# Performance work log

Measured on AMD Instinct MI355X. Metric: run time of the kernel, lower is better.

The kernel has to match this reference:

```python
import jax, jax.numpy as jnp
import numpy as np

B, Q, LE, D, P, A = 8, 32, 128, 512, 32, 128


def setup_inputs() -> dict:
    key = jax.random.key(0)
    ks = jax.random.split(key, 8)
    exp_tokens = jax.random.normal(ks[0], (B, Q, LE, D), dtype=jnp.float32)
    exp_mask = jax.random.randint(ks[1], (B, Q, LE), 0, 2, dtype=jnp.int32)
    s_j = jax.random.normal(ks[2], (B, P, D), dtype=jnp.float32)
    req_mask = jax.random.randint(ks[3], (B, P), 0, 2, dtype=jnp.int32)
    sc = 1.0 / np.sqrt(D)
    Ws_w = jax.random.normal(ks[4], (A, D), dtype=jnp.float32) * sc
    Ws_b = jax.random.normal(ks[5], (A,), dtype=jnp.float32) * 0.01
    U_w = jax.random.normal(ks[6], (A, D), dtype=jnp.float32) * sc
    v_w = jax.random.normal(ks[7], (1, A), dtype=jnp.float32) * (1.0 / np.sqrt(A))
    return {"exp_tokens": exp_tokens, "exp_mask": exp_mask, "s_j": s_j,
            "req_mask": req_mask, "Ws_w": Ws_w, "Ws_b": Ws_b, "U_w": U_w, "v_w": v_w}


def reference(exp_tokens, exp_mask, s_j, req_mask, Ws_w, Ws_b, U_w, v_w):
    # ws: (B,P,A); uh: (B,Q,Le,A)
    ws = jnp.einsum('bpd,ad->bpa', s_j, Ws_w) + Ws_b
    uh = jnp.einsum('bqtd,ad->bqta', exp_tokens, U_w)
    # broadcast add -> (B,Q,P,Le,A), tanh, project with v -> (B,Q,P,Le)
    scored = jnp.tanh(uh[:, :, None, :, :] + ws[:, None, :, None, :])
    e = jnp.einsum('bqpta,a->bqpt', scored, v_w[0])
    tok_mask = exp_mask[:, :, None, :]  # (B,Q,1,Le) broadcast over P
    e = jnp.where(tok_mask == 0, jnp.float32(-1e9), e)
    # joint softmax over Q*Le per (b,p)
    e_t = jnp.transpose(e, (0, 2, 1, 3)).reshape(e.shape[0], e.shape[2], -1)
    a = jax.nn.softmax(e_t, axis=-1).reshape(e.shape[0], e.shape[2], e.shape[1], e.shape[3])
    a = jnp.transpose(a, (0, 2, 1, 3))  # (B,Q,P,Le)
    s_rlk = jnp.einsum('bqpt,bqtd->bqpd', a, exp_tokens)
    rmask = req_mask[:, None, :, None].astype(s_rlk.dtype)
    return s_rlk * rmask
```

## Files before the change

### kernel.cpp

```cpp
#include <hip/hip_runtime.h>
#include <hip/hip_bf16.h>

#define B_  8
#define Q_  32
#define LE_ 128
#define D_  512
#define P_  32
#define A_  128

typedef __attribute__((ext_vector_type(8))) short short8_t;
typedef __attribute__((ext_vector_type(4))) float floatx4_t;

typedef const __attribute__((address_space(1))) unsigned int glb_uint;
typedef __attribute__((address_space(3))) unsigned int lds_uint;
#define GLD16(g, s) __builtin_amdgcn_global_load_lds((glb_uint*)(g), (lds_uint*)(s), 16, 0, 0)

__device__ __forceinline__ short f2bf(float x) {
    unsigned u = __float_as_uint(x);
    unsigned r = (u + 0x7fffu + ((u >> 16) & 1u)) >> 16;
    return (short)r;
}
__device__ __forceinline__ float bf2f(short s) {
    return __uint_as_float(((unsigned)(unsigned short)s) << 16);
}

__global__ __launch_bounds__(256) void convert_kernel(
    const float* __restrict__ X, const float* __restrict__ W,
    short* __restrict__ Xb, short* __restrict__ Wb) {
    int b = blockIdx.x;
    const float* src;
    short* dst;
    size_t base;
    if (b < 8192) {
        base = ((size_t)b * 256 + threadIdx.x) * 8;
        src = X + base; dst = Xb + base;
    } else {
        base = ((size_t)(b - 8192) * 256 + threadIdx.x) * 8;
        src = W + base; dst = Wb + base;
    }
    float4 v0 = ((const float4*)src)[0];
    float4 v1 = ((const float4*)src)[1];
    short8_t s;
    s[0] = f2bf(v0.x); s[1] = f2bf(v0.y); s[2] = f2bf(v0.z); s[3] = f2bf(v0.w);
    s[4] = f2bf(v1.x); s[5] = f2bf(v1.y); s[6] = f2bf(v1.z); s[7] = f2bf(v1.w);
    *(short8_t*)dst = s;
}

__global__ __launch_bounds__(128) void ws_kernel(
    const float* __restrict__ s_j, const float* __restrict__ Ws_w,
    const float* __restrict__ Ws_b, float* __restrict__ ws) {
    __shared__ float s_row[D_];
    int bp = blockIdx.x;
    const float* src = s_j + (size_t)bp * D_;
    for (int i = threadIdx.x; i < D_; i += 128) s_row[i] = src[i];
    __syncthreads();
    int a = threadIdx.x;
    const float4* w4 = (const float4*)(Ws_w + (size_t)a * D_);
    const float4* s4 = (const float4*)s_row;
    float acc = 0.0f;
#pragma unroll 8
    for (int i = 0; i < D_ / 4; ++i) {
        float4 w = w4[i];
        float4 s = s4[i];
        acc += w.x * s.x + w.y * s.y + w.z * s.z + w.w * s.w;
    }
    ws[bp * A_ + a] = __expf(2.0f * (acc + Ws_b[a]));
}

#define EUP_ 136
#define EWP_ 132
#define WPP_ 136

__global__ __launch_bounds__(512, 1) void fused_kernel(
    const short* __restrict__ Xb, const short* __restrict__ Wb,
    const float* __restrict__ EW, const float* __restrict__ v_w,
    const int* __restrict__ exp_mask, float* __restrict__ gsums,
    float* __restrict__ out) {
    __shared__ short uA[128 * EUP_];
    __shared__ float ew_s[32 * EWP_];
    __shared__ short w_s[32 * WPP_];
    __shared__ float n2v[128];
    __shared__ int   mask_s[128];

    int bq = blockIdx.x;
    int b  = bq >> 5;
    int tid = threadIdx.x;
    int wave = tid >> 6, lane = tid & 63;
    int qd = lane >> 4, lr = lane & 15;

    short* As = uA;
    short* Bs = uA + 8192;

    int m0 = (wave >> 1) * 32, n0 = (wave & 1) * 64;
    int cA = lane & 7;
    int row0 = wave * 16 + (lane >> 3);

    floatx4_t acc[2][4];
#pragma unroll
    for (int i = 0; i < 2; ++i)
#pragma unroll
        for (int j = 0; j < 4; ++j) acc[i][j] = (floatx4_t){0.f, 0.f, 0.f, 0.f};

    for (int kt = 0; kt < 8; ++kt) {
        int k0 = kt * 64;
        __syncthreads();
#pragma unroll
        for (int u = 0; u < 2; ++u) {
            int m = row0 + u * 8;
            GLD16(Xb + (size_t)(bq * 128 + m) * D_ + k0 + ((cA ^ (m & 7)) * 8),
                  As + (wave * 2 + u) * 512);
        }
#pragma unroll
        for (int u = 0; u < 2; ++u) {
            int n = row0 + u * 8;
            GLD16(Wb + (size_t)n * D_ + k0 + ((cA ^ (n & 7)) * 8),
                  Bs + (wave * 2 + u) * 512);
        }
        __syncthreads();
#pragma unroll
        for (int ks = 0; ks < 2; ++ks) {
            int cr = (ks * 4 + qd) ^ (lr & 7);
            short8_t af[2], bfr[4];
#pragma unroll
            for (int i = 0; i < 2; ++i)
                af[i] = *(const short8_t*)(As + (m0 + i * 16 + lr) * 64 + cr * 8);
#pragma unroll
            for (int j = 0; j < 4; ++j)
                bfr[j] = *(const short8_t*)(Bs + (n0 + j * 16 + lr) * 64 + cr * 8);
#pragma unroll
            for (int i = 0; i < 2; ++i)
#pragma unroll
                for (int j = 0; j < 4; ++j)
                    acc[i][j] = __builtin_amdgcn_mfma_f32_16x16x32_bf16(af[i], bfr[j], acc[i][j], 0, 0, 0);
        }
    }
    __syncthreads();

#pragma unroll
    for (int i = 0; i < 2; ++i)
#pragma unroll
        for (int j = 0; j < 4; ++j)
#pragma unroll
            for (int r = 0; r < 4; ++r) {
                int t = m0 + i * 16 + qd * 4 + r;
                int a = n0 + j * 16 + lr;
                uA[t * EUP_ + a] = f2bf(__expf(2.0f * acc[i][j][r]));
            }
#pragma unroll
    for (int u = 0; u < 2; ++u) {
        int c = tid * 2 + u;
        int p = c >> 5, seg = c & 31;
        *(float4*)&ew_s[p * EWP_ + seg * 4] =
            *(const float4*)&EW[(size_t)(b * P_ + p) * A_ + seg * 4];
    }
    if (tid < 32) {
        float4 v = *(const float4*)(v_w + tid * 4);
        v.x *= -2.0f; v.y *= -2.0f; v.z *= -2.0f; v.w *= -2.0f;
        *(float4*)&n2v[tid * 4] = v;
    }
    if (tid < 128) mask_s[tid] = exp_mask[bq * LE_ + tid];
    __syncthreads();

    {
        int t = tid & 127, pg = tid >> 7;
        float acc8[8];
#pragma unroll
        for (int j = 0; j < 8; ++j) acc8[j] = 0.0f;
        for (int a8 = 0; a8 < 16; ++a8) {
            short8_t e8 = *(const short8_t*)&uA[t * EUP_ + a8 * 8];
            float eu[8];
#pragma unroll
            for (int k = 0; k < 8; ++k) eu[k] = bf2f(e8[k]);
            float4 nv0 = *(const float4*)&n2v[a8 * 8];
            float4 nv1 = *(const float4*)&n2v[a8 * 8 + 4];
            float nv[8] = {nv0.x, nv0.y, nv0.z, nv0.w, nv1.x, nv1.y, nv1.z, nv1.w};
#pragma unroll
            for (int j = 0; j < 8; ++j) {
                int p = pg * 8 + j;
                float4 w0 = *(const float4*)&ew_s[p * EWP_ + a8 * 8];
                float4 w1 = *(const float4*)&ew_s[p * EWP_ + a8 * 8 + 4];
                float ww[8] = {w0.x, w0.y, w0.z, w0.w, w1.x, w1.y, w1.z, w1.w};
#pragma unroll
                for (int k = 0; k < 8; ++k)
                    acc8[j] = fmaf(nv[k], __builtin_amdgcn_rcpf(fmaf(eu[k], ww[k], 1.0f)), acc8[j]);
            }
        }
        int mk = mask_s[t];
#pragma unroll
        for (int j = 0; j < 8; ++j) {
            float ee = mk ? __expf(acc8[j]) : 0.0f;
            w_s[(pg * 8 + j) * WPP_ + t] = f2bf(ee);
        }
    }
    __syncthreads();

    if (tid < 256) {
        int p = tid >> 3, seg = tid & 7;
        const short* src = w_s + p * WPP_ + seg * 16;
        float s = 0.0f;
#pragma unroll
        for (int k = 0; k < 16; ++k) s += bf2f(src[k]);
        s += __shfl_xor(s, 1);
        s += __shfl_xor(s, 2);
        s += __shfl_xor(s, 4);
        if (seg == 0) atomicAdd(&gsums[b * P_ + p], s);
    }

    short8_t afv[2][4];
#pragma unroll
    for (int i = 0; i < 2; ++i)
#pragma unroll
        for (int ks = 0; ks < 4; ++ks)
            afv[i][ks] = *(const short8_t*)&w_s[(i * 16 + lr) * WPP_ + ks * 32 + qd * 8];

    int tt = tid >> 2, dseg = (tid & 3) * 32;
    for (int chunk = 0; chunk < 4; ++chunk) {
        int d0 = chunk * 128;
        __syncthreads();
        const short8_t* g = (const short8_t*)(Xb + (size_t)(bq * 128 + tt) * D_ + d0 + dseg);
        short8_t xs0 = g[0], xs1 = g[1], xs2 = g[2], xs3 = g[3];
#pragma unroll
        for (int e = 0; e < 8; ++e) {
            uA[(dseg + 0 + e) * EUP_ + tt]  = xs0[e];
            uA[(dseg + 8 + e) * EUP_ + tt]  = xs1[e];
            uA[(dseg + 16 + e) * EUP_ + tt] = xs2[e];
            uA[(dseg + 24 + e) * EUP_ + tt] = xs3[e];
        }
        __syncthreads();
        floatx4_t accp[2];
        accp[0] = (floatx4_t){0.f, 0.f, 0.f, 0.f};
        accp[1] = (floatx4_t){0.f, 0.f, 0.f, 0.f};
#pragma unroll
        for (int ks = 0; ks < 4; ++ks) {
            short8_t bfr = *(const short8_t*)&uA[(wave * 16 + lr) * EUP_ + ks * 32 + qd * 8];
            accp[0] = __builtin_amdgcn_mfma_f32_16x16x32_bf16(afv[0][ks], bfr, accp[0], 0, 0, 0);
            accp[1] = __builtin_amdgcn_mfma_f32_16x16x32_bf16(afv[1][ks], bfr, accp[1], 0, 0, 0);
        }
#pragma unroll
        for (int i = 0; i < 2; ++i)
#pragma unroll
            for (int r = 0; r < 4; ++r) {
                int p = i * 16 + qd * 4 + r;
                out[((size_t)bq * P_ + p) * D_ + d0 + wave * 16 + lr] = accp[i][r];
            }
    }
}

__global__ __launch_bounds__(256) void norm_kernel(
    float* __restrict__ out, const float* __restrict__ gsums,
    const int* __restrict__ req_mask) {
    int bqp = blockIdx.x;
    int p = bqp & 31;
    int b = bqp >> 10;
    int bp = b * P_ + p;
    float s = gsums[bp];
    float rm = req_mask[bp] ? __fdividef(1.0f, s) : 0.0f;
    float2* o = (float2*)(out + (size_t)bqp * D_);
    float2 v = o[threadIdx.x];
    v.x *= rm; v.y *= rm;
    o[threadIdx.x] = v;
}

extern "C" void kernel_launch(void* const* d_in, const int* in_sizes, int n_in,
                              void* d_out, int out_size, void* d_ws, size_t ws_size,
                              hipStream_t stream) {
    const float* exp_tokens = (const float*)d_in[0];
    const int*   exp_mask   = (const int*)d_in[1];
    const float* s_j        = (const float*)d_in[2];
    const int*   req_mask   = (const int*)d_in[3];
    const float* Ws_w       = (const float*)d_in[4];
    const float* Ws_b       = (const float*)d_in[5];
    const float* U_w        = (const float*)d_in[6];
    const float* v_w        = (const float*)d_in[7];
    float* out = (float*)d_out;

    float* EW    = (float*)d_ws;
    float* gsums = EW + B_ * P_ * A_;
    short* Xb    = (short*)(gsums + 256);
    short* Wb    = Xb + (size_t)B_ * Q_ * LE_ * D_;

    hipMemsetAsync(gsums, 0, B_ * P_ * sizeof(float), stream);
    convert_kernel<<<dim3(8192 + 32), dim3(256), 0, stream>>>(exp_tokens, U_w, Xb, Wb);
    ws_kernel<<<dim3(B_ * P_), dim3(128), 0, stream>>>(s_j, Ws_w, Ws_b, EW);
    fused_kernel<<<dim3(B_ * Q_), dim3(512), 0, stream>>>(Xb, Wb, EW, v_w, exp_mask, gsums, out);
    norm_kernel<<<dim3(B_ * Q_ * P_), dim3(256), 0, stream>>>(out, gsums, req_mask);
}
```

Before: 169.6 us.

## Fuse normalization into main kernel via cooperative grid sync

Removes the separate norm kernel: the fused kernel now performs a grid-wide cooperative sync after all blocks accumulate softmax denominators, reads the per-(b,p) sums, and scales the output by the reciprocal times the request mask before writing. Output stores become nontemporal. This saves a kernel launch and a full read-modify-write pass over the output, at the cost of a grid barrier that requires all 256 blocks to be co-resident.

```diff
diff --git a/kernel.cpp b/kernel.cpp
--- a/kernel.cpp
+++ b/kernel.cpp
@@ -1,5 +1,6 @@
 #include <hip/hip_runtime.h>
 #include <hip/hip_bf16.h>
+#include <hip/hip_cooperative_groups.h>
 
 #define B_  8
 #define Q_  32
@@ -75,7 +76,7 @@
     const short* __restrict__ Xb, const short* __restrict__ Wb,
     const float* __restrict__ EW, const float* __restrict__ v_w,
     const int* __restrict__ exp_mask, float* __restrict__ gsums,
-    float* __restrict__ out) {
+    const int* __restrict__ req_mask, float* __restrict__ out) {
     __shared__ short uA[128 * EUP_];
     __shared__ float ew_s[32 * EWP_];
     __shared__ short w_s[32 * WPP_];
@@ -213,6 +214,14 @@
         for (int ks = 0; ks < 4; ++ks)
             afv[i][ks] = *(const short8_t*)&w_s[(i * 16 + lr) * WPP_ + ks * 32 + qd * 8];
 
+    cooperative_groups::this_grid().sync();
+
+    if (tid < 32) {
+        int bp = b * P_ + tid;
+        float g = atomicAdd(&gsums[bp], 0.0f);
+        n2v[tid] = req_mask[bp] ? __builtin_amdgcn_rcpf(g) : 0.0f;
+    }
+
     int tt = tid >> 2, dseg = (tid & 3) * 32;
     for (int chunk = 0; chunk < 4; ++chunk) {
         int d0 = chunk * 128;
@@ -241,24 +250,12 @@
 #pragma unroll
             for (int r = 0; r < 4; ++r) {
                 int p = i * 16 + qd * 4 + r;
-                out[((size_t)bq * P_ + p) * D_ + d0 + wave * 16 + lr] = accp[i][r];
+                float rm = n2v[p];
+                __builtin_nontemporal_store(
+                    accp[i][r] * rm,
+                    &out[((size_t)bq * P_ + p) * D_ + d0 + wave * 16 + lr]);
             }
     }
-}
-
-__global__ __launch_bounds__(256) void norm_kernel(
-    float* __restrict__ out, const float* __restrict__ gsums,
-    const int* __restrict__ req_mask) {
-    int bqp = blockIdx.x;
-    int p = bqp & 31;
-    int b = bqp >> 10;
-    int bp = b * P_ + p;
-    float s = gsums[bp];
-    float rm = req_mask[bp] ? __fdividef(1.0f, s) : 0.0f;
-    float2* o = (float2*)(out + (size_t)bqp * D_);
-    float2 v = o[threadIdx.x];
-    v.x *= rm; v.y *= rm;
-    o[threadIdx.x] = v;
 }
 
 extern "C" void kernel_launch(void* const* d_in, const int* in_sizes, int n_in,
@@ -282,6 +279,14 @@
     hipMemsetAsync(gsums, 0, B_ * P_ * sizeof(float), stream);
     convert_kernel<<<dim3(8192 + 32), dim3(256), 0, stream>>>(exp_tokens, U_w, Xb, Wb);
     ws_kernel<<<dim3(B_ * P_), dim3(128), 0, stream>>>(s_j, Ws_w, Ws_b, EW);
-    fused_kernel<<<dim3(B_ * Q_), dim3(512), 0, stream>>>(Xb, Wb, EW, v_w, exp_mask, gsums, out);
-    norm_kernel<<<dim3(B_ * Q_ * P_), dim3(256), 0, stream>>>(out, gsums, req_mask);
-}
+
+    const short* Xb_c = Xb;
+    const short* Wb_c = Wb;
+    const float* EW_c = EW;
+    void* args[] = {
+        (void*)&Xb_c, (void*)&Wb_c, (void*)&EW_c, (void*)&v_w,
+        (void*)&exp_mask, (void*)&gsums, (void*)&req_mask, (void*)&out
+    };
+    hipLaunchCooperativeKernel((void*)fused_kernel, dim3(B_ * Q_), dim3(512),
+                               args, 0, stream);
+}
```

New measurement: 208.9 us. 23.1% more time.
